# Kernel optimization log

Hardware: AMD Instinct MI355X
Metric: run time of the kernel (lower is better)

The kernel has to match this reference:

```python
import jax, jax.numpy as jnp
import numpy as np

EPS = 1e-12  # torch F.normalize eps


def setup_inputs() -> dict:
    key = jax.random.key(0)
    k1, k2, k3 = jax.random.split(key, 3)
    b, c, h, w = 4, 192, 128, 128
    num_heads = 8
    in1 = jax.random.normal(k1, (b, c, h, w), dtype=jnp.float32)
    in2 = jax.random.normal(k2, (b, c, h, w), dtype=jnp.float32)
    scale = jnp.ones((num_heads, 1, 1), dtype=jnp.float32)
    proj_w = jax.random.normal(k3, (c, c), dtype=jnp.float32) * (1.0 / np.sqrt(c))
    return {"in1": in1, "in2": in2, "scale": scale, "proj_w": proj_w, "num_heads": num_heads}


def reference(in1, in2, scale, proj_w, num_heads):
    b, c, h, w = in1.shape
    hd = c // num_heads
    hw = h * w
    # b (head c) h w -> b head c (h w)
    q = in1.reshape(b, num_heads, hd, hw)
    k = in2.reshape(b, num_heads, hd, hw)
    # L2-normalize along the (h w) axis, torch eps semantics
    q = q / jnp.maximum(jnp.linalg.norm(q, axis=-1, keepdims=True), EPS)
    k = k / jnp.maximum(jnp.linalg.norm(k, axis=-1, keepdims=True), EPS)
    # channel-wise attention: [b, head, c, c]
    attn = jnp.einsum('bhcn,bhdn->bhcd', q, k) * scale  # scale broadcasts [head,1,1]
    attn = jax.nn.softmax(attn, axis=-1)
    out = jnp.einsum('bhcd,bhdn->bhcn', attn, k)
    out = out.reshape(b, c, h, w)
    # 1x1 conv projection (no bias)
    out = jnp.einsum('oc,bchw->bohw', proj_w, out)
    return out
```

## Files before the change

kernel.cpp:

```cpp
#include <hip/hip_runtime.h>
#include <hip/hip_bf16.h>
#include <math.h>

#define BATCH 4
#define NHEAD 8
#define HD 24
#define CH 192
#define HW 16384
#define NSPLIT 32

#define OFF_SQK 24576
#define OFF_S   49152
#define OFF_MO  638976
#define OFF_KT  712704

typedef __attribute__((ext_vector_type(8))) short bf16x8;
typedef __attribute__((ext_vector_type(4))) float f32x4;

__device__ __forceinline__ float dot4(const float4& a, const float4& b) {
    return fmaf(a.x, b.x, fmaf(a.y, b.y, fmaf(a.z, b.z, a.w * b.w)));
}

__device__ __forceinline__ unsigned short bf16rne(float x) {
    union { float f; unsigned u; } v; v.f = x;
    unsigned u = v.u;
    unsigned r = (u + 0x7FFFu + ((u >> 16) & 1u)) >> 16;
    return (unsigned short)r;
}

__device__ __forceinline__ bf16x8 pack8(const float4& a, const float4& b) {
    union { __hip_bfloat162 h; unsigned u; } c0, c1, c2, c3;
    c0.h = __float22bfloat162_rn(float2{a.x, a.y});
    c1.h = __float22bfloat162_rn(float2{a.z, a.w});
    c2.h = __float22bfloat162_rn(float2{b.x, b.y});
    c3.h = __float22bfloat162_rn(float2{b.z, b.w});
    union { unsigned u[4]; bf16x8 v; } r;
    r.u[0] = c0.u; r.u[1] = c1.u; r.u[2] = c2.u; r.u[3] = c3.u;
    return r.v;
}

__global__ __launch_bounds__(256) void kA(const float* __restrict__ q,
                                          const float* __restrict__ k,
                                          float* __restrict__ ws,
                                          unsigned short* __restrict__ kbfT) {
    const int bh   = blockIdx.x;
    const int sp   = blockIdx.y;
    const int t    = threadIdx.x;
    const int lane = t & 63;
    const int wave = t >> 6;
    const int nl   = lane & 15;
    const int quad = lane >> 4;
    const bool hiv = nl < 8;
    const int b    = bh >> 3;
    const int h    = bh & 7;

    const float* qb = q + (size_t)bh * HD * HW;
    const float* kb = k + (size_t)bh * HD * HW;
    unsigned short* kT = kbfT + (size_t)b * HW * CH + h * HD;

    f32x4 acc[2][2];
    #pragma unroll
    for (int mg = 0; mg < 2; ++mg)
        #pragma unroll
        for (int ng = 0; ng < 2; ++ng) acc[mg][ng] = (f32x4)(0.f);
    float sql = 0.f, sqh = 0.f, skl = 0.f, skh = 0.f;

    const int hwbase = sp * 512 + wave * 128;
    const float4 z4 = make_float4(0.f, 0.f, 0.f, 0.f);

    #pragma unroll 2
    for (int s = 0; s < 4; ++s) {
        const int off = hwbase + s * 32 + quad * 8;
        const float* qr = qb + (size_t)nl * HW + off;
        const float* kr = kb + (size_t)nl * HW + off;
        const float* qr2 = qb + (size_t)(16 + nl) * HW + off;
        const float* kr2 = kb + (size_t)(16 + nl) * HW + off;

        float4 q0 = *(const float4*)qr,  q1 = *(const float4*)(qr + 4);
        float4 k0 = *(const float4*)kr,  k1 = *(const float4*)(kr + 4);
        float4 q2 = hiv ? *(const float4*)qr2 : z4;
        float4 q3 = hiv ? *(const float4*)(qr2 + 4) : z4;
        float4 k2 = hiv ? *(const float4*)kr2 : z4;
        float4 k3 = hiv ? *(const float4*)(kr2 + 4) : z4;

        sql += dot4(q0, q0) + dot4(q1, q1);
        sqh += dot4(q2, q2) + dot4(q3, q3);
        skl += dot4(k0, k0) + dot4(k1, k1);
        skh += dot4(k2, k2) + dot4(k3, k3);

        bf16x8 aql = pack8(q0, q1), aqh = pack8(q2, q3);
        bf16x8 bkl = pack8(k0, k1), bkh = pack8(k2, k3);

        acc[0][0] = __builtin_amdgcn_mfma_f32_16x16x32_bf16(aql, bkl, acc[0][0], 0, 0, 0);
        acc[0][1] = __builtin_amdgcn_mfma_f32_16x16x32_bf16(aql, bkh, acc[0][1], 0, 0, 0);
        acc[1][0] = __builtin_amdgcn_mfma_f32_16x16x32_bf16(aqh, bkl, acc[1][0], 0, 0, 0);
        acc[1][1] = __builtin_amdgcn_mfma_f32_16x16x32_bf16(aqh, bkh, acc[1][1], 0, 0, 0);

        #pragma unroll
        for (int j = 0; j < 8; ++j)
            kT[(size_t)(off + j) * CH + nl] = (unsigned short)bkl[j];
        if (hiv) {
            #pragma unroll
            for (int j = 0; j < 8; ++j)
                kT[(size_t)(off + j) * CH + 16 + nl] = (unsigned short)bkh[j];
        }
    }

    sql += __shfl_xor(sql, 16, 64); sql += __shfl_xor(sql, 32, 64);
    sqh += __shfl_xor(sqh, 16, 64); sqh += __shfl_xor(sqh, 32, 64);
    skl += __shfl_xor(skl, 16, 64); skl += __shfl_xor(skl, 32, 64);
    skh += __shfl_xor(skh, 16, 64); skh += __shfl_xor(skh, 32, 64);

    __shared__ float red[4][576];
    __shared__ float rq[4][24], rk[4][24];
    if (lane < 16) { rq[wave][lane] = sql; rk[wave][lane] = skl; }
    if (lane < 8)  { rq[wave][16 + lane] = sqh; rk[wave][16 + lane] = skh; }

    #pragma unroll
    for (int mg = 0; mg < 2; ++mg)
        #pragma unroll
        for (int ng = 0; ng < 2; ++ng)
            #pragma unroll
            for (int r = 0; r < 4; ++r) {
                int i = mg * 16 + quad * 4 + r;
                int j = ng * 16 + nl;
                if (i < 24 && j < 24) red[wave][i * 24 + j] = acc[mg][ng][r];
            }
    __syncthreads();

    float* sqq = ws;
    float* sqk = ws + OFF_SQK;
    float* Sp  = ws + OFF_S;
    for (int e = t; e < 576; e += 256) {
        float v = red[0][e] + red[1][e] + red[2][e] + red[3][e];
        Sp[((size_t)bh * 576 + e) * NSPLIT + sp] = v;
    }
    if (t < 48) {
        int row = (t < 24) ? t : t - 24;
        float s;
        if (t < 24) s = rq[0][row] + rq[1][row] + rq[2][row] + rq[3][row];
        else        s = rk[0][row] + rk[1][row] + rk[2][row] + rk[3][row];
        float* dst = (t < 24) ? sqq : sqk;
        dst[(bh * HD + row) * NSPLIT + sp] = s;
    }
}

__global__ __launch_bounds__(256) void kB(const float* __restrict__ scale,
                                          const float* __restrict__ w,
                                          float* __restrict__ ws,
                                          unsigned short* __restrict__ Mo) {
    const int bh = blockIdx.x;
    const int b  = bh >> 3;
    const int h  = bh & 7;
    const int t  = threadIdx.x;

    __shared__ float qinv[HD], kinv[HD];
    __shared__ float A[HD * HD];
    __shared__ float wl[CH * HD];

    const float* sqq = ws;
    const float* sqk = ws + OFF_SQK;
    const float* Sp  = ws + OFF_S;

    if (t < 2 * HD) {
        const float* src = (t < HD) ? (sqq + (bh * HD + t) * NSPLIT)
                                    : (sqk + (bh * HD + (t - HD)) * NSPLIT);
        float4 s4 = make_float4(0.f, 0.f, 0.f, 0.f);
        #pragma unroll
        for (int i = 0; i < NSPLIT / 4; ++i) {
            float4 v = *(const float4*)(src + i * 4);
            s4.x += v.x; s4.y += v.y; s4.z += v.z; s4.w += v.w;
        }
        float s = s4.x + s4.y + s4.z + s4.w;
        float inv = 1.0f / fmaxf(sqrtf(s), 1e-12f);
        if (t < HD) qinv[t] = inv; else kinv[t - HD] = inv;
    }
    for (int idx = t; idx < CH * HD; idx += 256) {
        int o = idx / HD, dd = idx % HD;
        wl[idx] = w[o * CH + h * HD + dd];
    }
    __syncthreads();

    const float sc = scale[h];
    for (int e = t; e < HD * HD; e += 256) {
        const float* sp = Sp + ((size_t)bh * 576 + e) * NSPLIT;
        float4 s4 = make_float4(0.f, 0.f, 0.f, 0.f);
        #pragma unroll
        for (int i = 0; i < NSPLIT / 4; ++i) {
            float4 v = *(const float4*)(sp + i * 4);
            s4.x += v.x; s4.y += v.y; s4.z += v.z; s4.w += v.w;
        }
        float s = s4.x + s4.y + s4.z + s4.w;
        A[e] = s * qinv[e / HD] * kinv[e % HD] * sc;
    }
    __syncthreads();

    if (t < HD) {
        float m = -1e30f;
        for (int j = 0; j < HD; ++j) m = fmaxf(m, A[t * HD + j]);
        float sum = 0.f;
        for (int j = 0; j < HD; ++j) {
            float v = expf(A[t * HD + j] - m);
            A[t * HD + j] = v;
            sum += v;
        }
        float r = 1.0f / sum;
        for (int j = 0; j < HD; ++j) A[t * HD + j] *= r;
    }
    __syncthreads();

    for (int idx = t; idx < CH * HD; idx += 256) {
        int o = idx / HD, j = idx % HD;
        float v = 0.f;
        #pragma unroll
        for (int i = 0; i < HD; ++i) v = fmaf(wl[o * HD + i], A[i * HD + j], v);
        Mo[(size_t)b * CH * CH + (size_t)o * CH + h * HD + j] = bf16rne(v * kinv[j]);
    }
}

__global__ __launch_bounds__(256) void kC(const unsigned short* __restrict__ kbfT,
                                          const unsigned short* __restrict__ Mo,
                                          float* __restrict__ out) {
    const int t    = threadIdx.x;
    const int lane = t & 63;
    const int wave = t >> 6;
    const int nl   = lane & 15;
    const int quad = lane >> 4;

    const int nb = blockIdx.x * 128;
    const int ob = blockIdx.y * 64 + wave * 16;
    const int b  = blockIdx.z;

    const unsigned short* Arow = Mo + (size_t)b * CH * CH + (size_t)(ob + nl) * CH;
    const unsigned short* Kb   = kbfT + (size_t)b * HW * CH;

    f32x4 acc[8];
    #pragma unroll
    for (int nt = 0; nt < 8; ++nt) acc[nt] = (f32x4)(0.f);

    #pragma unroll 2
    for (int c0 = 0; c0 < CH; c0 += 32) {
        bf16x8 af = *(const bf16x8*)(Arow + c0 + quad * 8);
        #pragma unroll
        for (int nt = 0; nt < 8; ++nt) {
            bf16x8 bfv = *(const bf16x8*)(Kb + (size_t)(nb + nt * 16 + nl) * CH + c0 + quad * 8);
            acc[nt] = __builtin_amdgcn_mfma_f32_16x16x32_bf16(af, bfv, acc[nt], 0, 0, 0);
        }
    }

    float* op = out + (size_t)b * CH * HW;
    #pragma unroll
    for (int nt = 0; nt < 8; ++nt) {
        const int n = nb + nt * 16 + nl;
        #pragma unroll
        for (int r = 0; r < 4; ++r) {
            const int o = ob + quad * 4 + r;
            op[(size_t)o * HW + n] = acc[nt][r];
        }
    }
}

extern "C" void kernel_launch(void* const* d_in, const int* in_sizes, int n_in,
                              void* d_out, int out_size, void* d_ws, size_t ws_size,
                              hipStream_t stream) {
    const float* in1   = (const float*)d_in[0];
    const float* in2   = (const float*)d_in[1];
    const float* scale = (const float*)d_in[2];
    const float* projw = (const float*)d_in[3];
    float* ws  = (float*)d_ws;
    float* out = (float*)d_out;
    unsigned short* Mo   = (unsigned short*)(ws + OFF_MO);
    unsigned short* kbfT = (unsigned short*)(ws + OFF_KT);

    kA<<<dim3(32, NSPLIT), 256, 0, stream>>>(in1, in2, ws, kbfT);
    kB<<<32, 256, 0, stream>>>(scale, projw, ws, Mo);
    kC<<<dim3(HW / 128, CH / 64, BATCH), 256, 0, stream>>>(kbfT, Mo, out);
}
```

Before: 215.6 us.

## Drop transposed bf16 K buffer; convert K in projection kernel via LDS

The first kernel no longer writes a transposed bf16 copy of K. It instead uses 32x32x16 MFMAs with one wave per HW split, 128 splits, and writes the per-split Gram matrix and squared norms as contiguous rows. The projection kernel reads fp32 K directly, converts it to bf16 into an LDS tile, and computes 96 output channels per wave with 32x32 MFMAs. This removes the scattered 2-byte transpose stores and their read-back, at the cost of re-reading fp32 K and a larger partial-sum reduction in the middle kernel.

```diff
diff --git a/kernel.cpp b/kernel.cpp
--- a/kernel.cpp
+++ b/kernel.cpp
@@ -7,15 +7,14 @@
 #define HD 24
 #define CH 192
 #define HW 16384
-#define NSPLIT 32
-
-#define OFF_SQK 24576
-#define OFF_S   49152
-#define OFF_MO  638976
-#define OFF_KT  712704
-
-typedef __attribute__((ext_vector_type(8))) short bf16x8;
-typedef __attribute__((ext_vector_type(4))) float f32x4;
+#define SPL 128
+#define SPHW 128
+#define SROW 640
+
+#define OFF_MO (32 * SPL * SROW)
+
+typedef __attribute__((ext_vector_type(8)))  short bf16x8;
+typedef __attribute__((ext_vector_type(16))) float f32x16;
 
 __device__ __forceinline__ float dot4(const float4& a, const float4& b) {
     return fmaf(a.x, b.x, fmaf(a.y, b.y, fmaf(a.z, b.z, a.w * b.w)));
@@ -24,8 +23,7 @@
 __device__ __forceinline__ unsigned short bf16rne(float x) {
     union { float f; unsigned u; } v; v.f = x;
     unsigned u = v.u;
-    unsigned r = (u + 0x7FFFu + ((u >> 16) & 1u)) >> 16;
-    return (unsigned short)r;
+    return (unsigned short)((u + 0x7FFFu + ((u >> 16) & 1u)) >> 16);
 }
 
 __device__ __forceinline__ bf16x8 pack8(const float4& a, const float4& b) {
@@ -39,109 +37,54 @@
     return r.v;
 }
 
-__global__ __launch_bounds__(256) void kA(const float* __restrict__ q,
-                                          const float* __restrict__ k,
-                                          float* __restrict__ ws,
-                                          unsigned short* __restrict__ kbfT) {
+__global__ __launch_bounds__(128, 4) void kA(const float* __restrict__ q,
+                                             const float* __restrict__ k,
+                                             float* __restrict__ ws) {
     const int bh   = blockIdx.x;
-    const int sp   = blockIdx.y;
     const int t    = threadIdx.x;
+    const int wave = t >> 6;
     const int lane = t & 63;
-    const int wave = t >> 6;
-    const int nl   = lane & 15;
-    const int quad = lane >> 4;
-    const bool hiv = nl < 8;
-    const int b    = bh >> 3;
-    const int h    = bh & 7;
-
-    const float* qb = q + (size_t)bh * HD * HW;
-    const float* kb = k + (size_t)bh * HD * HW;
-    unsigned short* kT = kbfT + (size_t)b * HW * CH + h * HD;
-
-    f32x4 acc[2][2];
+    const int sp   = blockIdx.y * 2 + wave;
+    const int row  = lane & 31;
+    const int hi   = lane >> 5;
+    const bool rv  = row < HD;
+
+    const float* qb = q + (size_t)bh * HD * HW + (size_t)row * HW;
+    const float* kb = k + (size_t)bh * HD * HW + (size_t)row * HW;
+
+    f32x16 acc = {};
+    float sq = 0.f, sk = 0.f;
+    const int base = sp * SPHW + hi * 8;
+    const float4 z4 = make_float4(0.f, 0.f, 0.f, 0.f);
+
     #pragma unroll
-    for (int mg = 0; mg < 2; ++mg)
-        #pragma unroll
-        for (int ng = 0; ng < 2; ++ng) acc[mg][ng] = (f32x4)(0.f);
-    float sql = 0.f, sqh = 0.f, skl = 0.f, skh = 0.f;
-
-    const int hwbase = sp * 512 + wave * 128;
-    const float4 z4 = make_float4(0.f, 0.f, 0.f, 0.f);
-
-    #pragma unroll 2
-    for (int s = 0; s < 4; ++s) {
-        const int off = hwbase + s * 32 + quad * 8;
-        const float* qr = qb + (size_t)nl * HW + off;
-        const float* kr = kb + (size_t)nl * HW + off;
-        const float* qr2 = qb + (size_t)(16 + nl) * HW + off;
-        const float* kr2 = kb + (size_t)(16 + nl) * HW + off;
-
-        float4 q0 = *(const float4*)qr,  q1 = *(const float4*)(qr + 4);
-        float4 k0 = *(const float4*)kr,  k1 = *(const float4*)(kr + 4);
-        float4 q2 = hiv ? *(const float4*)qr2 : z4;
-        float4 q3 = hiv ? *(const float4*)(qr2 + 4) : z4;
-        float4 k2 = hiv ? *(const float4*)kr2 : z4;
-        float4 k3 = hiv ? *(const float4*)(kr2 + 4) : z4;
-
-        sql += dot4(q0, q0) + dot4(q1, q1);
-        sqh += dot4(q2, q2) + dot4(q3, q3);
-        skl += dot4(k0, k0) + dot4(k1, k1);
-        skh += dot4(k2, k2) + dot4(k3, k3);
-
-        bf16x8 aql = pack8(q0, q1), aqh = pack8(q2, q3);
-        bf16x8 bkl = pack8(k0, k1), bkh = pack8(k2, k3);
-
-        acc[0][0] = __builtin_amdgcn_mfma_f32_16x16x32_bf16(aql, bkl, acc[0][0], 0, 0, 0);
-        acc[0][1] = __builtin_amdgcn_mfma_f32_16x16x32_bf16(aql, bkh, acc[0][1], 0, 0, 0);
-        acc[1][0] = __builtin_amdgcn_mfma_f32_16x16x32_bf16(aqh, bkl, acc[1][0], 0, 0, 0);
-        acc[1][1] = __builtin_amdgcn_mfma_f32_16x16x32_bf16(aqh, bkh, acc[1][1], 0, 0, 0);
-
-        #pragma unroll
-        for (int j = 0; j < 8; ++j)
-            kT[(size_t)(off + j) * CH + nl] = (unsigned short)bkl[j];
-        if (hiv) {
-            #pragma unroll
-            for (int j = 0; j < 8; ++j)
-                kT[(size_t)(off + j) * CH + 16 + nl] = (unsigned short)bkh[j];
-        }
-    }
-
-    sql += __shfl_xor(sql, 16, 64); sql += __shfl_xor(sql, 32, 64);
-    sqh += __shfl_xor(sqh, 16, 64); sqh += __shfl_xor(sqh, 32, 64);
-    skl += __shfl_xor(skl, 16, 64); skl += __shfl_xor(skl, 32, 64);
-    skh += __shfl_xor(skh, 16, 64); skh += __shfl_xor(skh, 32, 64);
-
-    __shared__ float red[4][576];
-    __shared__ float rq[4][24], rk[4][24];
-    if (lane < 16) { rq[wave][lane] = sql; rk[wave][lane] = skl; }
-    if (lane < 8)  { rq[wave][16 + lane] = sqh; rk[wave][16 + lane] = skh; }
-
-    #pragma unroll
-    for (int mg = 0; mg < 2; ++mg)
-        #pragma unroll
-        for (int ng = 0; ng < 2; ++ng)
-            #pragma unroll
-            for (int r = 0; r < 4; ++r) {
-                int i = mg * 16 + quad * 4 + r;
-                int j = ng * 16 + nl;
-                if (i < 24 && j < 24) red[wave][i * 24 + j] = acc[mg][ng][r];
-            }
-    __syncthreads();
-
-    float* sqq = ws;
-    float* sqk = ws + OFF_SQK;
-    float* Sp  = ws + OFF_S;
-    for (int e = t; e < 576; e += 256) {
-        float v = red[0][e] + red[1][e] + red[2][e] + red[3][e];
-        Sp[((size_t)bh * 576 + e) * NSPLIT + sp] = v;
-    }
-    if (t < 48) {
-        int row = (t < 24) ? t : t - 24;
-        float s;
-        if (t < 24) s = rq[0][row] + rq[1][row] + rq[2][row] + rq[3][row];
-        else        s = rk[0][row] + rk[1][row] + rk[2][row] + rk[3][row];
-        float* dst = (t < 24) ? sqq : sqk;
-        dst[(bh * HD + row) * NSPLIT + sp] = s;
+    for (int s = 0; s < 8; ++s) {
+        const int off = base + s * 16;
+        float4 q0 = rv ? *(const float4*)(qb + off)     : z4;
+        float4 q1 = rv ? *(const float4*)(qb + off + 4) : z4;
+        float4 k0 = rv ? *(const float4*)(kb + off)     : z4;
+        float4 k1 = rv ? *(const float4*)(kb + off + 4) : z4;
+        sq += dot4(q0, q0) + dot4(q1, q1);
+        sk += dot4(k0, k0) + dot4(k1, k1);
+        bf16x8 aq = pack8(q0, q1);
+        bf16x8 bk = pack8(k0, k1);
+        acc = __builtin_amdgcn_mfma_f32_32x32x16_bf16(aq, bk, acc, 0, 0, 0);
+    }
+
+    sq += __shfl_xor(sq, 32, 64);
+    sk += __shfl_xor(sk, 32, 64);
+
+    float* Srow = ws + ((size_t)bh * SPL + sp) * SROW;
+    if (rv && hi == 0) {
+        Srow[576 + row] = sq;
+        Srow[600 + row] = sk;
+    }
+    if (row < HD) {
+        #pragma unroll
+        for (int r = 0; r < 16; ++r) {
+            int i = (r & 3) + 8 * (r >> 2) + 4 * hi;
+            if (i < HD) Srow[i * HD + row] = acc[r];
+        }
     }
 }
 
@@ -154,58 +97,52 @@
     const int h  = bh & 7;
     const int t  = threadIdx.x;
 
+    __shared__ float SA[624];
     __shared__ float qinv[HD], kinv[HD];
-    __shared__ float A[HD * HD];
     __shared__ float wl[CH * HD];
 
-    const float* sqq = ws;
-    const float* sqk = ws + OFF_SQK;
-    const float* Sp  = ws + OFF_S;
-
-    if (t < 2 * HD) {
-        const float* src = (t < HD) ? (sqq + (bh * HD + t) * NSPLIT)
-                                    : (sqk + (bh * HD + (t - HD)) * NSPLIT);
-        float4 s4 = make_float4(0.f, 0.f, 0.f, 0.f);
-        #pragma unroll
-        for (int i = 0; i < NSPLIT / 4; ++i) {
-            float4 v = *(const float4*)(src + i * 4);
-            s4.x += v.x; s4.y += v.y; s4.z += v.z; s4.w += v.w;
-        }
-        float s = s4.x + s4.y + s4.z + s4.w;
-        float inv = 1.0f / fmaxf(sqrtf(s), 1e-12f);
-        if (t < HD) qinv[t] = inv; else kinv[t - HD] = inv;
-    }
+    const float* base = ws + (size_t)bh * SPL * SROW;
+
+    float a0 = 0.f, a1 = 0.f, a2 = 0.f;
+    const int e0 = t, e1 = t + 256, e2 = t + 512;
+    for (int sp = 0; sp < SPL; ++sp) {
+        const float* r = base + (size_t)sp * SROW;
+        a0 += r[e0];
+        a1 += r[e1];
+        if (t < 112) a2 += r[e2];
+    }
+    SA[e0] = a0; SA[e1] = a1;
+    if (t < 112) SA[e2] = a2;
+
     for (int idx = t; idx < CH * HD; idx += 256) {
         int o = idx / HD, dd = idx % HD;
         wl[idx] = w[o * CH + h * HD + dd];
     }
     __syncthreads();
 
+    if (t < 2 * HD) {
+        float s = SA[576 + t];
+        float inv = 1.0f / fmaxf(sqrtf(s), 1e-12f);
+        if (t < HD) qinv[t] = inv; else kinv[t - HD] = inv;
+    }
+    __syncthreads();
+
     const float sc = scale[h];
-    for (int e = t; e < HD * HD; e += 256) {
-        const float* sp = Sp + ((size_t)bh * 576 + e) * NSPLIT;
-        float4 s4 = make_float4(0.f, 0.f, 0.f, 0.f);
-        #pragma unroll
-        for (int i = 0; i < NSPLIT / 4; ++i) {
-            float4 v = *(const float4*)(sp + i * 4);
-            s4.x += v.x; s4.y += v.y; s4.z += v.z; s4.w += v.w;
-        }
-        float s = s4.x + s4.y + s4.z + s4.w;
-        A[e] = s * qinv[e / HD] * kinv[e % HD] * sc;
-    }
+    for (int e = t; e < HD * HD; e += 256)
+        SA[e] = SA[e] * qinv[e / HD] * kinv[e % HD] * sc;
     __syncthreads();
 
     if (t < HD) {
         float m = -1e30f;
-        for (int j = 0; j < HD; ++j) m = fmaxf(m, A[t * HD + j]);
+        for (int j = 0; j < HD; ++j) m = fmaxf(m, SA[t * HD + j]);
         float sum = 0.f;
         for (int j = 0; j < HD; ++j) {
-            float v = expf(A[t * HD + j] - m);
-            A[t * HD + j] = v;
+            float v = expf(SA[t * HD + j] - m);
+            SA[t * HD + j] = v;
             sum += v;
         }
         float r = 1.0f / sum;
-        for (int j = 0; j < HD; ++j) A[t * HD + j] *= r;
+        for (int j = 0; j < HD; ++j) SA[t * HD + j] *= r;
     }
     __syncthreads();
 
@@ -213,51 +150,77 @@
         int o = idx / HD, j = idx % HD;
         float v = 0.f;
         #pragma unroll
-        for (int i = 0; i < HD; ++i) v = fmaf(wl[o * HD + i], A[i * HD + j], v);
+        for (int i = 0; i < HD; ++i) v = fmaf(wl[o * HD + i], SA[i * HD + j], v);
         Mo[(size_t)b * CH * CH + (size_t)o * CH + h * HD + j] = bf16rne(v * kinv[j]);
     }
 }
 
-__global__ __launch_bounds__(256) void kC(const unsigned short* __restrict__ kbfT,
-                                          const unsigned short* __restrict__ Mo,
-                                          float* __restrict__ out) {
+#define KCN 64
+#define BSTR 20
+
+__global__ __launch_bounds__(256, 4) void kC(const float* __restrict__ k,
+                                             const unsigned short* __restrict__ Mo,
+                                             float* __restrict__ out) {
+    __shared__ unsigned int Bt[KCN * BSTR];
+
     const int t    = threadIdx.x;
     const int lane = t & 63;
     const int wave = t >> 6;
-    const int nl   = lane & 15;
-    const int quad = lane >> 4;
-
-    const int nb = blockIdx.x * 128;
-    const int ob = blockIdx.y * 64 + wave * 16;
-    const int b  = blockIdx.z;
-
-    const unsigned short* Arow = Mo + (size_t)b * CH * CH + (size_t)(ob + nl) * CH;
-    const unsigned short* Kb   = kbfT + (size_t)b * HW * CH;
-
-    f32x4 acc[8];
+    const int n31  = lane & 31;
+    const int hi   = lane >> 5;
+    const int nt   = wave & 1;
+    const int otb  = (wave >> 1) * 3;
+
+    const int nb = blockIdx.x * KCN;
+    const int b  = blockIdx.y;
+
+    const float* kb = k + (size_t)b * CH * HW;
+    const unsigned short* Mob = Mo + (size_t)b * CH * CH;
+
+    const int sn = t & 63;
+    const int cq = t >> 6;
+
+    f32x16 acc[3] = {};
+
+    for (int c0 = 0; c0 < CH; c0 += 32) {
+        if (c0) __syncthreads();
+        float v[8];
+        #pragma unroll
+        for (int cc = 0; cc < 8; ++cc)
+            v[cc] = kb[(size_t)(c0 + cq * 8 + cc) * HW + nb + sn];
+        unsigned int wd[4];
+        #pragma unroll
+        for (int g = 0; g < 4; ++g) {
+            union { __hip_bfloat162 h; unsigned u; } cv;
+            cv.h = __float22bfloat162_rn(float2{v[2 * g], v[2 * g + 1]});
+            wd[g] = cv.u;
+        }
+        *(uint2*)&Bt[sn * BSTR + cq * 4]     = make_uint2(wd[0], wd[1]);
+        *(uint2*)&Bt[sn * BSTR + cq * 4 + 2] = make_uint2(wd[2], wd[3]);
+        __syncthreads();
+
+        #pragma unroll
+        for (int kc = 0; kc < 2; ++kc) {
+            bf16x8 Bf = *(const bf16x8*)&Bt[(nt * 32 + n31) * BSTR + kc * 8 + hi * 4];
+            #pragma unroll
+            for (int oi = 0; oi < 3; ++oi) {
+                const unsigned short* ap =
+                    Mob + (size_t)((otb + oi) * 32 + n31) * CH + c0 + kc * 16 + hi * 8;
+                bf16x8 Af = *(const bf16x8*)ap;
+                acc[oi] = __builtin_amdgcn_mfma_f32_32x32x16_bf16(Af, Bf, acc[oi], 0, 0, 0);
+            }
+        }
+    }
+
+    float* op = out + (size_t)b * CH * HW;
+    const int n = nb + nt * 32 + n31;
     #pragma unroll
-    for (int nt = 0; nt < 8; ++nt) acc[nt] = (f32x4)(0.f);
-
-    #pragma unroll 2
-    for (int c0 = 0; c0 < CH; c0 += 32) {
-        bf16x8 af = *(const bf16x8*)(Arow + c0 + quad * 8);
-        #pragma unroll
-        for (int nt = 0; nt < 8; ++nt) {
-            bf16x8 bfv = *(const bf16x8*)(Kb + (size_t)(nb + nt * 16 + nl) * CH + c0 + quad * 8);
-            acc[nt] = __builtin_amdgcn_mfma_f32_16x16x32_bf16(af, bfv, acc[nt], 0, 0, 0);
-        }
-    }
-
-    float* op = out + (size_t)b * CH * HW;
-    #pragma unroll
-    for (int nt = 0; nt < 8; ++nt) {
-        const int n = nb + nt * 16 + nl;
-        #pragma unroll
-        for (int r = 0; r < 4; ++r) {
-            const int o = ob + quad * 4 + r;
-            op[(size_t)o * HW + n] = acc[nt][r];
-        }
-    }
+    for (int oi = 0; oi < 3; ++oi)
+        #pragma unroll
+        for (int r = 0; r < 16; ++r) {
+            int o = (otb + oi) * 32 + (r & 3) + 8 * (r >> 2) + 4 * hi;
+            op[(size_t)o * HW + n] = acc[oi][r];
+        }
 }
 
 extern "C" void kernel_launch(void* const* d_in, const int* in_sizes, int n_in,
@@ -269,10 +232,9 @@
     const float* projw = (const float*)d_in[3];
     float* ws  = (float*)d_ws;
     float* out = (float*)d_out;
-    unsigned short* Mo   = (unsigned short*)(ws + OFF_MO);
-    unsigned short* kbfT = (unsigned short*)(ws + OFF_KT);
-
-    kA<<<dim3(32, NSPLIT), 256, 0, stream>>>(in1, in2, ws, kbfT);
+    unsigned short* Mo = (unsigned short*)(ws + OFF_MO);
+
+    kA<<<dim3(32, SPL / 2), 128, 0, stream>>>(in1, in2, ws);
     kB<<<32, 256, 0, stream>>>(scale, projw, ws, Mo);
-    kC<<<dim3(HW / 128, CH / 64, BATCH), 256, 0, stream>>>(kbfT, Mo, out);
-}
+    kC<<<dim3(HW / KCN, BATCH), 256, 0, stream>>>(in2, Mo, out);
+}
```

After: 261.3 us. 1.21x slower.
